# Kernel tuning notes

Hardware: AMD Instinct MI355X
Metric: run time of the kernel (lower is better)

## Reference

```python
import jax, jax.numpy as jnp
import numpy as np

B, L = 8, 16384
H = 64          # num_channel
N2 = 32         # s4_hidden_size // 2 complex conjugate-pair modes
DEPTH = 4       # model_depth
NLAYERS = 1 + DEPTH  # number of DSSM layers
EPS = 1e-5


def setup_inputs() -> dict:
    key = jax.random.key(0)
    ks = jax.random.split(key, 12)
    x = jax.random.normal(ks[0], (B, L), dtype=jnp.float32)
    # input linear 1 -> H
    w_in = jax.random.normal(ks[1], (H,), dtype=jnp.float32)
    b_in = jax.random.normal(ks[2], (H,), dtype=jnp.float32) * 0.1
    # hidden linears H -> H
    w_mid = jax.random.normal(ks[3], (DEPTH, H, H), dtype=jnp.float32) / np.sqrt(H)
    b_mid = jax.random.normal(ks[4], (DEPTH, H), dtype=jnp.float32) * 0.1
    # output linear H -> 1
    w_out = jax.random.normal(ks[5], (H,), dtype=jnp.float32) / np.sqrt(H)
    b_out = jax.random.normal(ks[6], (), dtype=jnp.float32) * 0.1
    # S4D / DSSM parameters (stacked over the 5 SSM layers)
    log_dt = (jax.random.uniform(ks[7], (NLAYERS, H), dtype=jnp.float32)
              * (np.log(0.1) - np.log(0.001)) + np.log(0.001))
    log_A_real = jnp.log(0.5 * jnp.ones((NLAYERS, H, N2), dtype=jnp.float32))
    A_imag = jnp.pi * jnp.broadcast_to(jnp.arange(N2, dtype=jnp.float32), (NLAYERS, H, N2))
    C_re = jax.random.normal(ks[8], (NLAYERS, H, N2), dtype=jnp.float32)
    C_im = jax.random.normal(ks[9], (NLAYERS, H, N2), dtype=jnp.float32)
    D = jax.random.normal(ks[10], (NLAYERS, H), dtype=jnp.float32)
    return {"x": x, "w_in": w_in, "b_in": b_in, "w_mid": w_mid, "b_mid": b_mid,
            "w_out": w_out, "b_out": b_out, "log_dt": log_dt,
            "log_A_real": log_A_real, "A_imag": A_imag,
            "C_re": C_re, "C_im": C_im, "D": D}


def _dssm(u, log_dt, log_A_real, A_imag, C_re, C_im, D):
    # u: [B, H, L]; diagonal SSM applied as FFT convolution (S4D ZOH kernel)
    Lq = u.shape[-1]
    dt = jnp.exp(log_dt)                      # [H]
    A = -jnp.exp(log_A_real) + 1j * A_imag    # [H, N2]
    dtA = A * dt[:, None]                     # [H, N2]
    C_eff = (C_re + 1j * C_im) * (jnp.exp(dtA) - 1.0) / A
    # Vandermonde: exp(dtA * l) for l in [0, L)
    V = jnp.exp(dtA[:, :, None] * jnp.arange(Lq, dtype=jnp.float32))  # [H, N2, L]
    k = 2.0 * jnp.einsum('hn,hnl->hl', C_eff, V).real                # [H, L]
    uf = jnp.fft.rfft(u, n=2 * Lq)
    kf = jnp.fft.rfft(k, n=2 * Lq)
    y = jnp.fft.irfft(uf * kf, n=2 * Lq)[..., :Lq]
    return y + u * D[:, None]


def reference(x, w_in, b_in, w_mid, b_mid, w_out, b_out,
              log_dt, log_A_real, A_imag, C_re, C_im, D):
    # side chain: Abs -> Decibel -> Linear(1,H) -> tanh -> [DSSM -> tanh] ...
    s = 20.0 * jnp.log10(jnp.abs(x) + EPS)            # [B, L]
    h = jnp.tanh(s[..., None] * w_in + b_in)          # [B, L, H]
    h = jnp.tanh(_dssm(h.transpose(0, 2, 1), log_dt[0], log_A_real[0],
                       A_imag[0], C_re[0], C_im[0], D[0]).transpose(0, 2, 1))
    for i in range(DEPTH):
        h = jnp.tanh(jnp.einsum('blh,oh->blo', h, w_mid[i]) + b_mid[i])
        j = i + 1
        h = jnp.tanh(_dssm(h.transpose(0, 2, 1), log_dt[j], log_A_real[j],
                           A_imag[j], C_re[j], C_im[j], D[j]).transpose(0, 2, 1))
    g = jnp.einsum('blh,h->bl', h, w_out) + b_out      # [B, L]
    g = jnp.power(10.0, g / 20.0)                      # Amplitude (dB -> linear)
    return x * g
```

## Files before the change

kernel.cpp:

```cpp
#include <hip/hip_runtime.h>
#include <math.h>

#define Bq 8
#define Lq 16384
#define Hq 64
#define N2q 32
#define NLAYERSq 5

typedef _Float16 f16x8 __attribute__((ext_vector_type(8)));
typedef _Float16 f16x4 __attribute__((ext_vector_type(4)));
typedef float    f32x4 __attribute__((ext_vector_type(4)));

#define MFMA16F(a, b, c) __builtin_amdgcn_mfma_f32_16x16x32_f16(a, b, c, 0, 0, 0)

#define UT_OFF    0
#define SS_OFF    32768
#define SMEM_SZ   50176
#define YST_OFF   0

#define WT_OFF_B   0
#define WP_OFF_B   163840
#define A2_OFF_B   (163840 + 5242880)
#define W16_OFF_B  (163840 + 5242880 + 15728640)
#define U_OFF_B    (163840 + 5242880 + 15728640 + 32768)

__device__ __forceinline__ float fast_tanh(float y) {
    float e = __expf(2.0f * y);
    return 1.0f - 2.0f * __builtin_amdgcn_rcpf(e + 1.0f);
}

__global__ __launch_bounds__(256)
void k_prep(const float* __restrict__ log_dt, const float* __restrict__ log_A_real,
            const float* __restrict__ A_imag, const float* __restrict__ C_re,
            const float* __restrict__ C_im, const float* __restrict__ Dvec,
            const float* __restrict__ w_mid,
            float* __restrict__ wT_tab, _Float16* __restrict__ Wp,
            _Float16* __restrict__ A2, _Float16* __restrict__ W16) {
    __shared__ float Pr[129][33], Pi[129][33];
    __shared__ float cre[32], cim[32], Kv[128];
    __shared__ double sdAr[32], sdAi[32];
    const int ph = blockIdx.x;
    const int tid = threadIdx.x;

    if (ph < 256 && tid < 64) {
        int e = ph * 64 + tid;
        W16[e] = (_Float16)w_mid[e];
    }

    if (tid < 32) {
        int n = tid;
        int pidx = ph * N2q + n;
        double dt  = exp((double)log_dt[ph]);
        double aRe = -exp((double)log_A_real[pidx]);
        double aIm = (double)A_imag[pidx];
        double dAr = aRe * dt, dAi = aIm * dt;
        sdAr[n] = dAr; sdAi[n] = dAi;
        double er  = exp(dAr);
        double wre = er * cos(dAi), wim = er * sin(dAi);
        double Er = wre - 1.0, Ei = wim;
        double inv = 1.0 / (aRe * aRe + aIm * aIm);
        double Fr = (Er * aRe + Ei * aIm) * inv;
        double Fi = (Ei * aRe - Er * aIm) * inv;
        double Cr = (double)C_re[pidx], Ci = (double)C_im[pidx];
        cre[n] = (float)(2.0 * (Cr * Fr - Ci * Fi));
        cim[n] = (float)(2.0 * (Cr * Fi + Ci * Fr));
        double qr = wre, qi = wim;
        #pragma unroll
        for (int s = 0; s < 7; s++) {
            double nr = qr * qr - qi * qi;
            qi = 2.0 * qr * qi; qr = nr;
        }
        float wTr = (float)qr, wTi = (float)qi;
        #pragma unroll
        for (int s = 0; s < 4; s++) {
            double nr = qr * qr - qi * qi;
            qi = 2.0 * qr * qi; qr = nr;
        }
        float* wt = wT_tab + ph * 128 + n * 4;
        wt[0] = wTr; wt[1] = wTi; wt[2] = (float)qr; wt[3] = (float)qi;
    }
    __syncthreads();

    const double TWO_PI  = 6.2831853071795864769;
    const double INV_2PI = 0.15915494309189533577;
    for (int e = tid; e < 129 * 32; e += 256) {
        int j = e >> 5, n = e & 31;
        double phd = (double)j * sdAi[n];
        double r   = fma(-TWO_PI, nearbyint(phd * INV_2PI), phd);
        float  mag = __expf((float)((double)j * sdAr[n]));
        float  rf  = (float)r;
        Pr[j][n] = mag * cosf(rf);
        Pi[j][n] = mag * sinf(rf);
    }
    __syncthreads();

    if (tid < 128) {
        int d = tid;
        float s = 0.f;
        #pragma unroll 8
        for (int n = 0; n < 32; n++)
            s += cre[n] * Pr[d][n] - cim[n] * Pi[d][n];
        if (d == 0) s += Dvec[ph];
        Kv[d] = s;
    }
    __syncthreads();

    _Float16* wpb = Wp + (size_t)ph * 8192;
    for (int e = tid; e < 8192; e += 256) {
        int kk = e >> 7, l = e & 127;
        float v = (kk < 32) ? Pr[127 - l][kk] : Pi[127 - l][kk - 32];
        wpb[e] = (_Float16)v;
    }
    _Float16* a2b = A2 + (size_t)ph * 24576;
    for (int e = tid; e < 24576; e += 256) {
        int m = e / 192, k = e - m * 192;
        float v;
        if (k < 128) {
            v = (k <= m) ? Kv[m - k] : 0.f;
        } else {
            int kk = k - 128, n2 = kk & 31;
            float pr = Pr[m + 1][n2], pi2 = Pi[m + 1][n2];
            v = (kk < 32) ? (cre[n2] * pr - cim[n2] * pi2)
                          : -(cre[n2] * pi2 + cim[n2] * pr);
        }
        a2b[e] = (_Float16)v;
    }
}

__global__ __launch_bounds__(256, 3)
void k_scan(const float* __restrict__ x, _Float16* __restrict__ u16,
            const _Float16* __restrict__ Wp_all, const _Float16* __restrict__ A2_all,
            const float* __restrict__ wT_all, int layer,
            const float* __restrict__ w_in, const float* __restrict__ b_in) {
    extern __shared__ char smem[];
    char* UT = smem + UT_OFF;
    char* Sf = smem + SS_OFF;
    char* St = smem + SS_OFF;
    char* yst = smem + YST_OFF;

    const int bh = blockIdx.x;
    const int h  = bh & 63;
    const int tid = threadIdx.x;
    const int lane = tid & 63;
    const int wave = tid >> 6;
    const int ph = layer * 64 + h;
    const _Float16* Wp = Wp_all + (size_t)ph * 8192;
    const _Float16* A2 = A2_all + (size_t)ph * 24576;
    const float* wT4 = wT_all + ph * 128;
    _Float16* uu = u16 + ((size_t)bh << 14);

    const int rA = lane & 15;
    const int qA = lane >> 4;

    if (layer == 0) {
        const float* xb = x + ((size_t)(bh >> 6) << 14);
        const float wi = w_in[h], bi = b_in[h];
        for (int it = 0; it < 8; ++it) {
            int flat8 = (it * 256 + tid) * 8;
            int n = flat8 >> 7, k = flat8 & 127;
            float4 a = *(const float4*)(xb + flat8);
            float4 b = *(const float4*)(xb + flat8 + 4);
            float f[8] = {a.x, a.y, a.z, a.w, b.x, b.y, b.z, b.w};
            f16x8 hv;
            #pragma unroll
            for (int j = 0; j < 8; j++) {
                float s = 6.0205999132796239f * __log2f(fabsf(f[j]) + 1e-5f);
                hv[j] = (_Float16)fast_tanh(fmaf(s, wi, bi));
            }
            *(f16x8*)(UT + n * 256 + ((k * 2) ^ ((n & 7) << 4))) = hv;
        }
    } else {
        for (int it = 0; it < 8; ++it) {
            int flat8 = (it * 256 + tid) * 8;
            int n = flat8 >> 7, k = flat8 & 127;
            f16x8 hv = *(const f16x8*)(uu + flat8);
            *(f16x8*)(UT + n * 256 + ((k * 2) ^ ((n & 7) << 4))) = hv;
        }
    }
    __syncthreads();

    {
        f32x4 acc1[8];
        #pragma unroll
        for (int nt = 0; nt < 8; nt++) acc1[nt] = (f32x4){0.f, 0.f, 0.f, 0.f};
        for (int ks = 0; ks < 4; ks++) {
            f16x8 af = *(const f16x8*)(Wp + (wave * 16 + rA) * 128 + ks * 32 + qA * 8);
            #pragma unroll
            for (int nt = 0; nt < 8; nt++) {
                int n = nt * 16 + rA;
                f16x8 bv = *(const f16x8*)(UT + n * 256 + ((ks * 64 + qA * 16) ^ ((n & 7) << 4)));
                acc1[nt] = MFMA16F(af, bv, acc1[nt]);
            }
        }
        #pragma unroll
        for (int nt = 0; nt < 8; nt++) {
            int c = nt * 16 + rA;
            #pragma unroll
            for (int r = 0; r < 4; r++)
                *(_Float16*)(Sf + (wave * 16 + qA * 4 + r) * 272 + c * 2) = (_Float16)acc1[nt][r];
        }
    }
    __syncthreads();

    {
        const int sn = tid >> 3;
        const int ss = tid & 7;
        const float wTr = wT4[sn * 4 + 0], wTi = wT4[sn * 4 + 1];
        float fr[16], fi[16];
        {
            f16x8 a0 = *(const f16x8*)(Sf + sn * 272 + ss * 32);
            f16x8 a1 = *(const f16x8*)(Sf + sn * 272 + ss * 32 + 16);
            f16x8 b0 = *(const f16x8*)(Sf + (sn + 32) * 272 + ss * 32);
            f16x8 b1 = *(const f16x8*)(Sf + (sn + 32) * 272 + ss * 32 + 16);
            #pragma unroll
            for (int j = 0; j < 8; j++) {
                fr[j] = (float)a0[j]; fr[j + 8] = (float)a1[j];
                fi[j] = (float)b0[j]; fi[j + 8] = (float)b1[j];
            }
        }
        float Tr = 0.f, Ti = 0.f;
        #pragma unroll
        for (int i = 0; i < 16; i++) {
            float nTr = fmaf(wTr, Tr, fmaf(-wTi, Ti, fr[i]));
            Ti = fmaf(wTr, Ti, fmaf(wTi, Tr, fi[i]));
            Tr = nTr;
        }
        float gr = wT4[sn * 4 + 2], gi = wT4[sn * 4 + 3];
        #pragma unroll
        for (int s = 0; s < 3; s++) {
            float pr = __shfl_up(Tr, 1 << s, 8);
            float pi = __shfl_up(Ti, 1 << s, 8);
            if (ss >= (1 << s)) {
                Tr = fmaf(gr, pr, fmaf(-gi, pi, Tr));
                Ti = fmaf(gr, pi, fmaf(gi, pr, Ti));
            }
            float ngr = fmaf(gr, gr, -gi * gi);
            gi = 2.f * gr * gi; gr = ngr;
        }
        float Er_ = __shfl_up(Tr, 1, 8);
        float Ei_ = __shfl_up(Ti, 1, 8);
        if (ss == 0) { Er_ = 0.f; Ei_ = 0.f; }
        __syncthreads();
        float Gr = Er_, Gi = Ei_;
        #pragma unroll
        for (int i = 0; i < 16; i++) {
            int c = ss * 16 + i;
            int sw = (c & 7) << 4;
            *(_Float16*)(St + c * 128 + ((sn * 2) ^ sw))        = (_Float16)Gr;
            *(_Float16*)(St + c * 128 + (((sn + 32) * 2) ^ sw)) = (_Float16)Gi;
            float nGr = fmaf(wTr, Gr, fmaf(-wTi, Gi, fr[i]));
            Gi = fmaf(wTr, Gi, fmaf(wTi, Gr, fi[i]));
            Gr = nGr;
        }
    }
    __syncthreads();

    f32x4 acc[2][8];
    #pragma unroll
    for (int mi = 0; mi < 2; mi++)
        #pragma unroll
        for (int nt = 0; nt < 8; nt++) acc[mi][nt] = (f32x4){0.f, 0.f, 0.f, 0.f};
    #pragma unroll
    for (int mi = 0; mi < 2; mi++) {
        const _Float16* Arow = A2 + ((wave * 2 + mi) * 16 + rA) * 192;
        for (int ks = 0; ks < 4; ks++) {
            f16x8 af = *(const f16x8*)(Arow + ks * 32 + qA * 8);
            #pragma unroll
            for (int nt = 0; nt < 8; nt++) {
                int n = nt * 16 + rA;
                f16x8 bv = *(const f16x8*)(UT + n * 256 + ((ks * 64 + qA * 16) ^ ((n & 7) << 4)));
                acc[mi][nt] = MFMA16F(af, bv, acc[mi][nt]);
            }
        }
        #pragma unroll
        for (int ks2 = 0; ks2 < 2; ks2++) {
            f16x8 af = *(const f16x8*)(Arow + 128 + ks2 * 32 + qA * 8);
            #pragma unroll
            for (int nt = 0; nt < 8; nt++) {
                int c = nt * 16 + rA;
                f16x8 bv = *(const f16x8*)(St + c * 128 + ((ks2 * 64 + qA * 16) ^ ((c & 7) << 4)));
                acc[mi][nt] = MFMA16F(af, bv, acc[mi][nt]);
            }
        }
    }
    __syncthreads();

    #pragma unroll
    for (int mi = 0; mi < 2; mi++) {
        int m0 = (wave * 2 + mi) * 16 + qA * 4;
        #pragma unroll
        for (int nt = 0; nt < 8; nt++) {
            int c = nt * 16 + rA;
            f16x4 o;
            o[0] = (_Float16)fast_tanh(acc[mi][nt][0]);
            o[1] = (_Float16)fast_tanh(acc[mi][nt][1]);
            o[2] = (_Float16)fast_tanh(acc[mi][nt][2]);
            o[3] = (_Float16)fast_tanh(acc[mi][nt][3]);
            *(f16x4*)(yst + c * 272 + m0 * 2) = o;
        }
    }
    __syncthreads();
    for (int it = 0; it < 8; ++it) {
        int e = it * 256 + tid;
        int c = e >> 4, l8 = e & 15;
        f16x8 hv = *(const f16x8*)(yst + c * 272 + l8 * 16);
        *(f16x8*)(uu + c * 128 + l8 * 8) = hv;
    }
}

__global__ __launch_bounds__(256, 4)
void k_linear(_Float16* __restrict__ uio, const _Float16* __restrict__ W16,
              const float* __restrict__ bias) {
    __shared__ __align__(16) char lmem[33792];
    _Float16* Ul  = (_Float16*)lmem;
    _Float16* yst = (_Float16*)lmem;

    const int b   = blockIdx.y;
    const int l0  = blockIdx.x * 256;
    const int tid = threadIdx.x;
    const int lane = tid & 63;
    const int wave = tid >> 6;
    const int rA = lane & 15;
    const int qA = lane >> 4;

    _Float16* ub = uio + ((size_t)b << 20) + l0;

    for (int it = 0; it < 4; ++it) {
        int g  = it * 256 + tid;
        int hp = g >> 5;
        int l8 = g & 31;
        f16x8 v0 = *(const f16x8*)(ub + (size_t)(hp * 2)     * Lq + l8 * 8);
        f16x8 v1 = *(const f16x8*)(ub + (size_t)(hp * 2 + 1) * Lq + l8 * 8);
        const unsigned short* p0 = (const unsigned short*)&v0;
        const unsigned short* p1 = (const unsigned short*)&v1;
        int sw = (l8 & 7) << 4;
        #pragma unroll
        for (int j = 0; j < 8; j++) {
            unsigned int pk = (unsigned int)p0[j] | ((unsigned int)p1[j] << 16);
            *(unsigned int*)((char*)Ul + (l8 * 8 + j) * 128 + ((hp * 4) ^ sw)) = pk;
        }
    }
    __syncthreads();

    f32x4 acc[16];
    #pragma unroll
    for (int nt = 0; nt < 16; nt++) acc[nt] = (f32x4){0.f, 0.f, 0.f, 0.f};
    const _Float16* Wrow = W16 + (wave * 16 + rA) * 64;
    #pragma unroll
    for (int kf = 0; kf < 2; kf++) {
        f16x8 af = *(const f16x8*)(Wrow + kf * 32 + qA * 8);
        #pragma unroll
        for (int nt = 0; nt < 16; nt++) {
            int n = nt * 16 + rA;
            int sw = ((n >> 3) & 7) << 4;
            f16x8 bv = *(const f16x8*)((char*)Ul + n * 128 + ((kf * 64 + qA * 16) ^ sw));
            acc[nt] = MFMA16F(af, bv, acc[nt]);
        }
    }
    __syncthreads();

    {
        int ob = wave * 16 + qA * 4;
        float bo0 = bias[ob], bo1 = bias[ob + 1], bo2 = bias[ob + 2], bo3 = bias[ob + 3];
        #pragma unroll
        for (int nt = 0; nt < 16; nt++) {
            int l = nt * 16 + rA;
            yst[(ob + 0) * 264 + l] = (_Float16)fast_tanh(acc[nt][0] + bo0);
            yst[(ob + 1) * 264 + l] = (_Float16)fast_tanh(acc[nt][1] + bo1);
            yst[(ob + 2) * 264 + l] = (_Float16)fast_tanh(acc[nt][2] + bo2);
            yst[(ob + 3) * 264 + l] = (_Float16)fast_tanh(acc[nt][3] + bo3);
        }
    }
    __syncthreads();
    for (int it = 0; it < 8; ++it) {
        int e = it * 256 + tid;
        int o = e >> 5, l8 = e & 31;
        f16x8 hv = *(const f16x8*)(yst + o * 264 + l8 * 8);
        *(f16x8*)(ub + (size_t)o * Lq + l8 * 8) = hv;
    }
}

__global__ __launch_bounds__(256)
void k_out(const _Float16* __restrict__ u16, const float* __restrict__ x,
           const float* __restrict__ w_out, const float* __restrict__ b_out,
           float* __restrict__ out) {
    int idx = blockIdx.x * 256 + threadIdx.x;
    int b = idx >> 14;
    int l = idx & (Lq - 1);
    const _Float16* up = u16 + ((size_t)b << 20) + l;
    float acc = 0.f;
    #pragma unroll 8
    for (int hh = 0; hh < 64; ++hh)
        acc = fmaf(w_out[hh], (float)up[(size_t)hh << 14], acc);
    float g = acc + b_out[0];
    out[idx] = x[idx] * exp2f(g * 0.16609640474436812f);
}

extern "C" void kernel_launch(void* const* d_in, const int* in_sizes, int n_in,
                              void* d_out, int out_size, void* d_ws, size_t ws_size,
                              hipStream_t stream) {
    const float* x          = (const float*)d_in[0];
    const float* w_in       = (const float*)d_in[1];
    const float* b_in       = (const float*)d_in[2];
    const float* w_mid      = (const float*)d_in[3];
    const float* b_mid      = (const float*)d_in[4];
    const float* w_out      = (const float*)d_in[5];
    const float* b_out      = (const float*)d_in[6];
    const float* log_dt     = (const float*)d_in[7];
    const float* log_A_real = (const float*)d_in[8];
    const float* A_imag     = (const float*)d_in[9];
    const float* C_re       = (const float*)d_in[10];
    const float* C_im       = (const float*)d_in[11];
    const float* Dv         = (const float*)d_in[12];

    char* ws = (char*)d_ws;
    float*     wT_tab = (float*)(ws + WT_OFF_B);
    _Float16*  Wp     = (_Float16*)(ws + WP_OFF_B);
    _Float16*  A2     = (_Float16*)(ws + A2_OFF_B);
    _Float16*  W16    = (_Float16*)(ws + W16_OFF_B);
    _Float16*  u16    = (_Float16*)(ws + U_OFF_B);
    float* out = (float*)d_out;

    hipFuncSetAttribute((const void*)k_scan,
                        hipFuncAttributeMaxDynamicSharedMemorySize, SMEM_SZ);

    k_prep<<<NLAYERSq * Hq, 256, 0, stream>>>(log_dt, log_A_real, A_imag,
                                              C_re, C_im, Dv, w_mid,
                                              wT_tab, Wp, A2, W16);
    for (int layer = 0; layer < NLAYERSq; layer++) {
        if (layer > 0)
            k_linear<<<dim3(Lq / 256, Bq), 256, 0, stream>>>(
                u16, W16 + (size_t)(layer - 1) * Hq * Hq, b_mid + (size_t)(layer - 1) * Hq);
        k_scan<<<Bq * Hq, 256, SMEM_SZ, stream>>>(x, u16, Wp, A2, wT_tab, layer,
                                                  w_in, b_in);
    }
    k_out<<<(Bq * Lq) / 256, 256, 0, stream>>>(u16, x, w_out, b_out, out);
}
```

Measured before the change: 176.7 us.

## Fuse intra-chunk Toeplitz GEMM with state GEMM and write output directly

New measurement: 184.7 us. 4.5% more time.

```diff
diff --git a/kernel.cpp b/kernel.cpp
--- a/kernel.cpp
+++ b/kernel.cpp
@@ -16,13 +16,12 @@
 #define UT_OFF    0
 #define SS_OFF    32768
 #define SMEM_SZ   50176
-#define YST_OFF   0
 
 #define WT_OFF_B   0
-#define WP_OFF_B   163840
-#define A2_OFF_B   (163840 + 5242880)
-#define W16_OFF_B  (163840 + 5242880 + 15728640)
-#define U_OFF_B    (163840 + 5242880 + 15728640 + 32768)
+#define AT_OFF_B   163840
+#define ET_OFF_B   (163840 + 15728640)
+#define W16_OFF_B  (163840 + 15728640 + 5242880)
+#define U_OFF_B    (163840 + 15728640 + 5242880 + 32768)
 
 __device__ __forceinline__ float fast_tanh(float y) {
     float e = __expf(2.0f * y);
@@ -34,8 +33,8 @@
             const float* __restrict__ A_imag, const float* __restrict__ C_re,
             const float* __restrict__ C_im, const float* __restrict__ Dvec,
             const float* __restrict__ w_mid,
-            float* __restrict__ wT_tab, _Float16* __restrict__ Wp,
-            _Float16* __restrict__ A2, _Float16* __restrict__ W16) {
+            float* __restrict__ wT_tab, _Float16* __restrict__ At,
+            _Float16* __restrict__ Et, _Float16* __restrict__ W16) {
     __shared__ float Pr[129][33], Pi[129][33];
     __shared__ float cre[32], cim[32], Kv[128];
     __shared__ double sdAr[32], sdAi[32];
@@ -105,38 +104,38 @@
     }
     __syncthreads();
 
-    _Float16* wpb = Wp + (size_t)ph * 8192;
+    _Float16* atb = At + (size_t)ph * 24576;
+    for (int e = tid; e < 24576; e += 256) {
+        int r = e >> 7, k = e & 127;
+        float v;
+        if (r < 64) {
+            v = (r < 32) ? Pr[127 - k][r] : Pi[127 - k][r - 32];
+        } else {
+            int m = r - 64;
+            v = (k <= m) ? Kv[m - k] : 0.f;
+        }
+        atb[e] = (_Float16)v;
+    }
+    _Float16* etb = Et + (size_t)ph * 8192;
     for (int e = tid; e < 8192; e += 256) {
-        int kk = e >> 7, l = e & 127;
-        float v = (kk < 32) ? Pr[127 - l][kk] : Pi[127 - l][kk - 32];
-        wpb[e] = (_Float16)v;
-    }
-    _Float16* a2b = A2 + (size_t)ph * 24576;
-    for (int e = tid; e < 24576; e += 256) {
-        int m = e / 192, k = e - m * 192;
-        float v;
-        if (k < 128) {
-            v = (k <= m) ? Kv[m - k] : 0.f;
-        } else {
-            int kk = k - 128, n2 = kk & 31;
-            float pr = Pr[m + 1][n2], pi2 = Pi[m + 1][n2];
-            v = (kk < 32) ? (cre[n2] * pr - cim[n2] * pi2)
-                          : -(cre[n2] * pi2 + cim[n2] * pr);
-        }
-        a2b[e] = (_Float16)v;
+        int m = e >> 6, kk = e & 63;
+        int n2 = kk & 31;
+        float pr = Pr[m + 1][n2], pi2 = Pi[m + 1][n2];
+        float v = (kk < 32) ? (cre[n2] * pr - cim[n2] * pi2)
+                            : -(cre[n2] * pi2 + cim[n2] * pr);
+        etb[e] = (_Float16)v;
     }
 }
 
 __global__ __launch_bounds__(256, 3)
 void k_scan(const float* __restrict__ x, _Float16* __restrict__ u16,
-            const _Float16* __restrict__ Wp_all, const _Float16* __restrict__ A2_all,
+            const _Float16* __restrict__ At_all, const _Float16* __restrict__ Et_all,
             const float* __restrict__ wT_all, int layer,
             const float* __restrict__ w_in, const float* __restrict__ b_in) {
     extern __shared__ char smem[];
     char* UT = smem + UT_OFF;
     char* Sf = smem + SS_OFF;
     char* St = smem + SS_OFF;
-    char* yst = smem + YST_OFF;
 
     const int bh = blockIdx.x;
     const int h  = bh & 63;
@@ -144,8 +143,8 @@
     const int lane = tid & 63;
     const int wave = tid >> 6;
     const int ph = layer * 64 + h;
-    const _Float16* Wp = Wp_all + (size_t)ph * 8192;
-    const _Float16* A2 = A2_all + (size_t)ph * 24576;
+    const _Float16* At = At_all + (size_t)ph * 24576;
+    const _Float16* Et = Et_all + (size_t)ph * 8192;
     const float* wT4 = wT_all + ph * 128;
     _Float16* uu = u16 + ((size_t)bh << 14);
 
@@ -179,26 +178,33 @@
     }
     __syncthreads();
 
-    {
-        f32x4 acc1[8];
-        #pragma unroll
-        for (int nt = 0; nt < 8; nt++) acc1[nt] = (f32x4){0.f, 0.f, 0.f, 0.f};
-        for (int ks = 0; ks < 4; ks++) {
-            f16x8 af = *(const f16x8*)(Wp + (wave * 16 + rA) * 128 + ks * 32 + qA * 8);
-            #pragma unroll
-            for (int nt = 0; nt < 8; nt++) {
-                int n = nt * 16 + rA;
-                f16x8 bv = *(const f16x8*)(UT + n * 256 + ((ks * 64 + qA * 16) ^ ((n & 7) << 4)));
-                acc1[nt] = MFMA16F(af, bv, acc1[nt]);
-            }
-        }
+    f32x4 accS[8];
+    f32x4 accY[2][8];
+    #pragma unroll
+    for (int nt = 0; nt < 8; nt++) {
+        accS[nt]    = (f32x4){0.f, 0.f, 0.f, 0.f};
+        accY[0][nt] = (f32x4){0.f, 0.f, 0.f, 0.f};
+        accY[1][nt] = (f32x4){0.f, 0.f, 0.f, 0.f};
+    }
+    for (int ks = 0; ks < 4; ks++) {
+        f16x8 aS  = *(const f16x8*)(At + (wave * 16 + rA) * 128 + ks * 32 + qA * 8);
+        f16x8 aY0 = *(const f16x8*)(At + (64 + (wave * 2 + 0) * 16 + rA) * 128 + ks * 32 + qA * 8);
+        f16x8 aY1 = *(const f16x8*)(At + (64 + (wave * 2 + 1) * 16 + rA) * 128 + ks * 32 + qA * 8);
         #pragma unroll
         for (int nt = 0; nt < 8; nt++) {
-            int c = nt * 16 + rA;
-            #pragma unroll
-            for (int r = 0; r < 4; r++)
-                *(_Float16*)(Sf + (wave * 16 + qA * 4 + r) * 272 + c * 2) = (_Float16)acc1[nt][r];
-        }
+            int n = nt * 16 + rA;
+            f16x8 bv = *(const f16x8*)(UT + n * 256 + ((ks * 64 + qA * 16) ^ ((n & 7) << 4)));
+            accS[nt]    = MFMA16F(aS,  bv, accS[nt]);
+            accY[0][nt] = MFMA16F(aY0, bv, accY[0][nt]);
+            accY[1][nt] = MFMA16F(aY1, bv, accY[1][nt]);
+        }
+    }
+    #pragma unroll
+    for (int nt = 0; nt < 8; nt++) {
+        int c = nt * 16 + rA;
+        #pragma unroll
+        for (int r = 0; r < 4; r++)
+            *(_Float16*)(Sf + (wave * 16 + qA * 4 + r) * 272 + c * 2) = (_Float16)accS[nt][r];
     }
     __syncthreads();
 
@@ -255,56 +261,30 @@
     }
     __syncthreads();
 
-    f32x4 acc[2][8];
-    #pragma unroll
-    for (int mi = 0; mi < 2; mi++)
-        #pragma unroll
-        for (int nt = 0; nt < 8; nt++) acc[mi][nt] = (f32x4){0.f, 0.f, 0.f, 0.f};
     #pragma unroll
     for (int mi = 0; mi < 2; mi++) {
-        const _Float16* Arow = A2 + ((wave * 2 + mi) * 16 + rA) * 192;
-        for (int ks = 0; ks < 4; ks++) {
-            f16x8 af = *(const f16x8*)(Arow + ks * 32 + qA * 8);
-            #pragma unroll
-            for (int nt = 0; nt < 8; nt++) {
-                int n = nt * 16 + rA;
-                f16x8 bv = *(const f16x8*)(UT + n * 256 + ((ks * 64 + qA * 16) ^ ((n & 7) << 4)));
-                acc[mi][nt] = MFMA16F(af, bv, acc[mi][nt]);
-            }
-        }
+        const _Float16* Erow = Et + ((wave * 2 + mi) * 16 + rA) * 64;
         #pragma unroll
         for (int ks2 = 0; ks2 < 2; ks2++) {
-            f16x8 af = *(const f16x8*)(Arow + 128 + ks2 * 32 + qA * 8);
+            f16x8 af = *(const f16x8*)(Erow + ks2 * 32 + qA * 8);
             #pragma unroll
             for (int nt = 0; nt < 8; nt++) {
                 int c = nt * 16 + rA;
                 f16x8 bv = *(const f16x8*)(St + c * 128 + ((ks2 * 64 + qA * 16) ^ ((c & 7) << 4)));
-                acc[mi][nt] = MFMA16F(af, bv, acc[mi][nt]);
+                accY[mi][nt] = MFMA16F(af, bv, accY[mi][nt]);
             }
         }
-    }
-    __syncthreads();
-
-    #pragma unroll
-    for (int mi = 0; mi < 2; mi++) {
         int m0 = (wave * 2 + mi) * 16 + qA * 4;
         #pragma unroll
         for (int nt = 0; nt < 8; nt++) {
             int c = nt * 16 + rA;
             f16x4 o;
-            o[0] = (_Float16)fast_tanh(acc[mi][nt][0]);
-            o[1] = (_Float16)fast_tanh(acc[mi][nt][1]);
-            o[2] = (_Float16)fast_tanh(acc[mi][nt][2]);
-            o[3] = (_Float16)fast_tanh(acc[mi][nt][3]);
-            *(f16x4*)(yst + c * 272 + m0 * 2) = o;
-        }
-    }
-    __syncthreads();
-    for (int it = 0; it < 8; ++it) {
-        int e = it * 256 + tid;
-        int c = e >> 4, l8 = e & 15;
-        f16x8 hv = *(const f16x8*)(yst + c * 272 + l8 * 16);
-        *(f16x8*)(uu + c * 128 + l8 * 8) = hv;
+            o[0] = (_Float16)fast_tanh(accY[mi][nt][0]);
+            o[1] = (_Float16)fast_tanh(accY[mi][nt][1]);
+            o[2] = (_Float16)fast_tanh(accY[mi][nt][2]);
+            o[3] = (_Float16)fast_tanh(accY[mi][nt][3]);
+            *(f16x4*)(uu + c * 128 + m0) = o;
+        }
     }
 }
 
@@ -415,8 +395,8 @@
 
     char* ws = (char*)d_ws;
     float*     wT_tab = (float*)(ws + WT_OFF_B);
-    _Float16*  Wp     = (_Float16*)(ws + WP_OFF_B);
-    _Float16*  A2     = (_Float16*)(ws + A2_OFF_B);
+    _Float16*  At     = (_Float16*)(ws + AT_OFF_B);
+    _Float16*  Et     = (_Float16*)(ws + ET_OFF_B);
     _Float16*  W16    = (_Float16*)(ws + W16_OFF_B);
     _Float16*  u16    = (_Float16*)(ws + U_OFF_B);
     float* out = (float*)d_out;
@@ -426,12 +406,12 @@
 
     k_prep<<<NLAYERSq * Hq, 256, 0, stream>>>(log_dt, log_A_real, A_imag,
                                               C_re, C_im, Dv, w_mid,
-                                              wT_tab, Wp, A2, W16);
+                                              wT_tab, At, Et, W16);
     for (int layer = 0; layer < NLAYERSq; layer++) {
         if (layer > 0)
             k_linear<<<dim3(Lq / 256, Bq), 256, 0, stream>>>(
                 u16, W16 + (size_t)(layer - 1) * Hq * Hq, b_mid + (size_t)(layer - 1) * Hq);
-        k_scan<<<Bq * Hq, 256, SMEM_SZ, stream>>>(x, u16, Wp, A2, wT_tab, layer,
+        k_scan<<<Bq * Hq, 256, SMEM_SZ, stream>>>(x, u16, At, Et, wT_tab, layer,
                                                   w_in, b_in);
     }
     k_out<<<(Bq * Lq) / 256, 256, 0, stream>>>(u16, x, w_out, b_out, out);
```
